# Kernel tuning notes

Hardware: AMD Instinct MI355X
Metric: run time of the kernel (lower is better)

## Reference

```python
import jax, jax.numpy as jnp
import numpy as np
import math

EMB, SEQ, OUT, FF, B = 1024, 1024, 2, 1024, 32
EPS = 1e-5


def _build_pe(seq_len, emb_dim):
    # Faithful to the buggy torch loop: for even i, pe[pos,i] is first set to sin
    # then immediately overwritten by cos(pos / 10000**(2*(i+1)/emb_dim));
    # odd indices are never written (stay 0).
    pos = np.arange(seq_len, dtype=np.float64)[:, None]
    i = np.arange(0, emb_dim, 2, dtype=np.float64)[None, :]
    pe = np.zeros((seq_len, emb_dim), dtype=np.float32)
    pe[:, ::2] = np.cos(pos / 10000.0 ** (2.0 * (i + 1.0) / emb_dim)).astype(np.float32)
    return jnp.asarray(pe)[None]  # [1, S, D]


def setup_inputs() -> dict:
    key = jax.random.key(0)
    ks = jax.random.split(key, 24)
    std = 0.02
    W = lambda k, o, i: jax.random.normal(k, (o, i), jnp.float32) * std
    b = lambda k, o: jax.random.normal(k, (o,), jnp.float32) * std
    return {
        "x": jax.random.normal(ks[0], (B, SEQ, EMB), jnp.float32),
        "pe": _build_pe(SEQ, EMB),
        "ln1_g": jnp.ones((EMB,), jnp.float32), "ln1_b": jnp.zeros((EMB,), jnp.float32),
        "Wq": W(ks[1], EMB, EMB), "bq": b(ks[2], EMB),
        "Wk": W(ks[3], EMB, EMB), "bk": b(ks[4], EMB),
        "Wv": W(ks[5], EMB, EMB), "bv": b(ks[6], EMB),
        "Wo": W(ks[7], EMB, EMB), "bo": b(ks[8], EMB),
        "ln2_g": jnp.ones((EMB,), jnp.float32), "ln2_b": jnp.zeros((EMB,), jnp.float32),
        "W1": W(ks[9], FF, EMB), "b1": b(ks[10], FF),
        "W2": W(ks[11], EMB, FF), "b2": b(ks[12], EMB),
        "Wc": W(ks[13], OUT, EMB), "bc": b(ks[14], OUT),
    }


def _ln(x, g, bias):
    mu = jnp.mean(x, axis=-1, keepdims=True)
    var = jnp.mean(jnp.square(x - mu), axis=-1, keepdims=True)
    return (x - mu) * jax.lax.rsqrt(var + EPS) * g + bias


def _block(x, ln1_g, ln1_b, Wq, bq, Wk, bk, Wv, bv, Wo, bo, ln2_g, ln2_b, W1, b1, W2, b2):
    h = _ln(x, ln1_g, ln1_b)
    q = h @ Wq.T + bq
    k = h @ Wk.T + bk
    v = h @ Wv.T + bv
    scores = jnp.einsum('bqd,bkd->bqk', q, k) / math.sqrt(EMB)
    w = jax.nn.softmax(scores, axis=-1)  # [B,S,S]
    attn = jnp.einsum('bqk,bkd->bqd', w, v) @ Wo.T + bo
    x2 = x + attn  # dropout is identity in eval
    h2 = _ln(x2, ln2_g, ln2_b)
    ff = jax.nn.relu(h2 @ W1.T + b1) @ W2.T + b2
    return x2 + ff, w


def reference(x, pe, ln1_g, ln1_b, Wq, bq, Wk, bk, Wv, bv, Wo, bo, ln2_g, ln2_b, W1, b1, W2, b2, Wc, bc):
    x1 = math.sqrt(EMB) * x + pe
    # Original forward applies block net2_1 twice (net2_2 is unused) -> reuse params.
    p = (ln1_g, ln1_b, Wq, bq, Wk, bk, Wv, bv, Wo, bo, ln2_g, ln2_b, W1, b1, W2, b2)
    x2_1, w1 = _block(x1, *p)
    x2_2, w2 = _block(x2_1, *p)
    logits = x2_2[:, 0, :] @ Wc.T + bc
    return logits, w1, w2
```

## Files before the change

kernel.cpp:

```cpp
#include <hip/hip_runtime.h>
#include <cstdint>


#define AS1 __attribute__((address_space(1)))
#define AS3 __attribute__((address_space(3)))

typedef __attribute__((ext_vector_type(8))) short bf16x8;
typedef __attribute__((ext_vector_type(4))) float f32x4;
typedef __attribute__((ext_vector_type(4))) unsigned short us4;

__device__ __forceinline__ unsigned short f2bf(float f) {
  unsigned int u = __builtin_bit_cast(unsigned int, f);
  u += 0x7fffu + ((u >> 16) & 1u);
  return (unsigned short)(u >> 16);
}
__device__ __forceinline__ float bf2f(unsigned short h) {
  return __builtin_bit_cast(float, (unsigned int)h << 16);
}

__device__ __forceinline__ void gload_lds16(const void* g, void* l) {
  auto gp = reinterpret_cast<AS1 unsigned int*>(reinterpret_cast<uintptr_t>(g));
  auto lp = reinterpret_cast<AS3 unsigned int*>(reinterpret_cast<uintptr_t>(l));
  __builtin_amdgcn_global_load_lds(gp, lp, 16, 0, 0);
}

enum { M_BF16 = 0, M_RELU = 1, M_QKV = 2, M_SCBF = 3, M_RESID = 4 };

template<int MODE>
__global__ __launch_bounds__(256, 3) void gemm_bt(
    const unsigned short* __restrict__ A, long long sAb,
    const unsigned short* __restrict__ B, long long sBb,
    const float* __restrict__ bias,
    const float* __restrict__ resid,
    float* __restrict__ outF,
    unsigned short* __restrict__ outBF,
    long long sOb, int N, int K, float scale)
{
  __shared__ __align__(16) unsigned short As[128 * 64];
  __shared__ __align__(16) unsigned short Bs[128 * 64];
  const int t    = threadIdx.x;
  const int w    = t >> 6;
  const int lane = t & 63;
  const int quad = lane >> 4;
  const int l16  = lane & 15;
  const int bz   = blockIdx.z;
  const unsigned short* Ab = A + (long long)bz * sAb;
  const unsigned short* Bb = B + (long long)bz * sBb;
  const int m0 = blockIdx.y * 128;
  const int n0 = blockIdx.x * 128;
  const int srow = t >> 3;
  const int scol = (t & 7) * 8;
  const int wr = (w >> 1) * 64;
  const int wc = (w & 1) * 64;

  const f32x4 zero = {0.f, 0.f, 0.f, 0.f};
  f32x4 acc[4][4];
#pragma unroll
  for (int i = 0; i < 4; ++i)
#pragma unroll
    for (int j = 0; j < 4; ++j) acc[i][j] = zero;

  for (int k0 = 0; k0 < K; k0 += 64) {
#pragma unroll
    for (int c = 0; c < 4; ++c) {
      gload_lds16(Ab + (long long)(m0 + c * 32 + srow) * K + (k0 + scol),
                  As + c * 2048 + w * 512);
      gload_lds16(Bb + (long long)(n0 + c * 32 + srow) * K + (k0 + scol),
                  Bs + c * 2048 + w * 512);
    }
    __syncthreads();
#pragma unroll
    for (int kk = 0; kk < 64; kk += 32) {
      bf16x8 af[4], bfr[4];
#pragma unroll
      for (int i = 0; i < 4; ++i)
        af[i] = *(const bf16x8*)&As[(wr + i * 16 + l16) * 64 + kk + quad * 8];
#pragma unroll
      for (int j = 0; j < 4; ++j)
        bfr[j] = *(const bf16x8*)&Bs[(wc + j * 16 + l16) * 64 + kk + quad * 8];
#pragma unroll
      for (int i = 0; i < 4; ++i)
#pragma unroll
        for (int j = 0; j < 4; ++j)
          acc[i][j] = __builtin_amdgcn_mfma_f32_16x16x32_bf16(af[i], bfr[j], acc[i][j], 0, 0, 0);
    }
    __syncthreads();
  }

#pragma unroll
  for (int i = 0; i < 4; ++i) {
#pragma unroll
    for (int j = 0; j < 4; ++j) {
      const int mt = m0 + wr + i * 16 + quad * 4;
      const int nt = n0 + wc + j * 16 + l16;
      f32x4 d = acc[i][j];
      if (MODE == M_BF16 || MODE == M_RELU) {
        const float bv = bias ? bias[nt] : 0.0f;
#pragma unroll
        for (int r = 0; r < 4; ++r) {
          float v = d[r] + bv;
          if (MODE == M_RELU) v = fmaxf(v, 0.0f);
          outBF[(long long)bz * sOb + (long long)(mt + r) * N + nt] = f2bf(v);
        }
      } else if (MODE == M_SCBF) {
#pragma unroll
        for (int r = 0; r < 4; ++r)
          outBF[(long long)bz * sOb + (long long)(mt + r) * N + nt] = f2bf(d[r] * scale);
      } else if (MODE == M_RESID) {
        const float bv = bias[nt];
#pragma unroll
        for (int r = 0; r < 4; ++r) {
          const long long idx = (long long)(mt + r) * N + nt;
          outF[idx] = resid[idx] + d[r] + bv;
        }
      } else if (MODE == M_QKV) {
        const int seg = n0 >> 10;
        const int ntl = nt - (seg << 10);
        const float bv = bias[nt];
        if (seg < 2) {
          unsigned short* dst = outBF + (long long)seg * 33554432LL;
#pragma unroll
          for (int r = 0; r < 4; ++r)
            dst[(long long)(mt + r) * 1024 + ntl] = f2bf(d[r] + bv);
        } else {
          unsigned short* dst = outBF + 2LL * 33554432LL;
          us4 pk;
#pragma unroll
          for (int r = 0; r < 4; ++r) pk[r] = f2bf(d[r] + bv);
          const int b = mt >> 10;
          const int s = mt & 1023;
          *(us4*)&dst[(long long)b * 1048576 + (long long)ntl * 1024 + s] = pk;
        }
      }
    }
  }
}

template<int EMBED>
__global__ __launch_bounds__(256) void ln_kernel(
    const float* __restrict__ xin, const float* __restrict__ pe,
    float* __restrict__ x1out,
    const float* __restrict__ g, const float* __restrict__ bb,
    unsigned short* __restrict__ hout)
{
  __shared__ float red[8];
  const long long row = blockIdx.x;
  const int t = threadIdx.x, lane = t & 63, w = t >> 6;
  float4 v = *(const float4*)(xin + row * 1024 + t * 4);
  if (EMBED) {
    const int s = (int)(row & 1023);
    float4 p = *(const float4*)(pe + (long long)s * 1024 + t * 4);
    v.x = 32.0f * v.x + p.x;
    v.y = 32.0f * v.y + p.y;
    v.z = 32.0f * v.z + p.z;
    v.w = 32.0f * v.w + p.w;
    *(float4*)(x1out + row * 1024 + t * 4) = v;
  }
  float sum = v.x + v.y + v.z + v.w;
  float sq  = v.x * v.x + v.y * v.y + v.z * v.z + v.w * v.w;
#pragma unroll
  for (int off = 32; off > 0; off >>= 1) {
    sum += __shfl_down(sum, off, 64);
    sq  += __shfl_down(sq,  off, 64);
  }
  if (lane == 0) { red[w] = sum; red[4 + w] = sq; }
  __syncthreads();
  sum = red[0] + red[1] + red[2] + red[3];
  sq  = red[4] + red[5] + red[6] + red[7];
  const float mu  = sum * (1.0f / 1024.0f);
  const float var = sq * (1.0f / 1024.0f) - mu * mu;
  const float rs  = rsqrtf(var + 1e-5f);
  float4 gg = *(const float4*)(g + t * 4);
  float4 bv = *(const float4*)(bb + t * 4);
  us4 h;
  h[0] = f2bf((v.x - mu) * rs * gg.x + bv.x);
  h[1] = f2bf((v.y - mu) * rs * gg.y + bv.y);
  h[2] = f2bf((v.z - mu) * rs * gg.z + bv.z);
  h[3] = f2bf((v.w - mu) * rs * gg.w + bv.w);
  *(us4*)(hout + row * 1024 + t * 4) = h;
}

__global__ __launch_bounds__(256) void softmax_kernel(
    const unsigned short* __restrict__ sbf,
    float* __restrict__ wout, unsigned short* __restrict__ wbf)
{
  __shared__ float red[8];
  const long long row = blockIdx.x;
  const int t = threadIdx.x, lane = t & 63, w = t >> 6;
  us4 sv = *(const us4*)(sbf + row * 1024 + t * 4);
  float4 v;
  v.x = bf2f(sv[0]); v.y = bf2f(sv[1]); v.z = bf2f(sv[2]); v.w = bf2f(sv[3]);
  float mx = fmaxf(fmaxf(v.x, v.y), fmaxf(v.z, v.w));
#pragma unroll
  for (int off = 32; off > 0; off >>= 1) mx = fmaxf(mx, __shfl_down(mx, off, 64));
  if (lane == 0) red[w] = mx;
  __syncthreads();
  mx = fmaxf(fmaxf(red[0], red[1]), fmaxf(red[2], red[3]));
  __syncthreads();
  const float e0 = __expf(v.x - mx), e1 = __expf(v.y - mx);
  const float e2 = __expf(v.z - mx), e3 = __expf(v.w - mx);
  float s = e0 + e1 + e2 + e3;
#pragma unroll
  for (int off = 32; off > 0; off >>= 1) s += __shfl_down(s, off, 64);
  if (lane == 0) red[w] = s;
  __syncthreads();
  s = red[0] + red[1] + red[2] + red[3];
  const float inv = 1.0f / s;
  float4 o; o.x = e0 * inv; o.y = e1 * inv; o.z = e2 * inv; o.w = e3 * inv;
  *(float4*)(wout + row * 1024 + t * 4) = o;
  us4 ob;
  ob[0] = f2bf(o.x); ob[1] = f2bf(o.y); ob[2] = f2bf(o.z); ob[3] = f2bf(o.w);
  *(us4*)(wbf + row * 1024 + t * 4) = ob;
}

__global__ __launch_bounds__(256) void prep_kernel(
    const float* __restrict__ Wq, const float* __restrict__ Wk, const float* __restrict__ Wv,
    const float* __restrict__ Wo, const float* __restrict__ W1, const float* __restrict__ W2,
    const float* __restrict__ bq, const float* __restrict__ bk, const float* __restrict__ bv,
    unsigned short* __restrict__ qkvw, unsigned short* __restrict__ Wo_bf,
    unsigned short* __restrict__ W1_bf, unsigned short* __restrict__ W2_bf,
    float* __restrict__ qkvb)
{
  const int y = blockIdx.y;
  const long long i = blockIdx.x * 256 + threadIdx.x;
  if (y == 6) {
    if (i < 768) {
      const float* src = (i < 256) ? bq : (i < 512) ? bk : bv;
      float4 v = *(const float4*)(src + (i & 255) * 4);
      *(float4*)(qkvb + i * 4) = v;
    }
    return;
  }
  const float* src;
  unsigned short* dst;
  switch (y) {
    case 0: src = Wq; dst = qkvw;            break;
    case 1: src = Wk; dst = qkvw + 1048576;  break;
    case 2: src = Wv; dst = qkvw + 2097152;  break;
    case 3: src = Wo; dst = Wo_bf;           break;
    case 4: src = W1; dst = W1_bf;           break;
    default: src = W2; dst = W2_bf;          break;
  }
  float4 v = *(const float4*)(src + i * 4);
  us4 o;
  o[0] = f2bf(v.x); o[1] = f2bf(v.y); o[2] = f2bf(v.z); o[3] = f2bf(v.w);
  *(us4*)(dst + i * 4) = o;
}

__global__ __launch_bounds__(256) void logits_kernel(
    const float* __restrict__ x, const float* __restrict__ Wc,
    const float* __restrict__ bc, float* __restrict__ out)
{
  __shared__ float red[4];
  const int blk = blockIdx.x;
  const int b = blk >> 1, o = blk & 1;
  const int t = threadIdx.x, lane = t & 63, w = t >> 6;
  const float* xr = x + (long long)b * 1048576;
  const float* wr = Wc + o * 1024;
  float4 xv = *(const float4*)(xr + t * 4);
  float4 wv = *(const float4*)(wr + t * 4);
  float s = xv.x * wv.x + xv.y * wv.y + xv.z * wv.z + xv.w * wv.w;
#pragma unroll
  for (int off = 32; off > 0; off >>= 1) s += __shfl_down(s, off, 64);
  if (lane == 0) red[w] = s;
  __syncthreads();
  if (t == 0) out[blk] = red[0] + red[1] + red[2] + red[3] + bc[o];
}

extern "C" void kernel_launch(void* const* d_in, const int* in_sizes, int n_in,
                              void* d_out, int out_size, void* d_ws, size_t ws_size,
                              hipStream_t stream)
{
  const float* x    = (const float*)d_in[0];
  const float* pe   = (const float*)d_in[1];
  const float* ln1g = (const float*)d_in[2];
  const float* ln1b = (const float*)d_in[3];
  const float* Wq   = (const float*)d_in[4];
  const float* bq   = (const float*)d_in[5];
  const float* Wk   = (const float*)d_in[6];
  const float* bk   = (const float*)d_in[7];
  const float* Wv   = (const float*)d_in[8];
  const float* bv   = (const float*)d_in[9];
  const float* Wo   = (const float*)d_in[10];
  const float* bo   = (const float*)d_in[11];
  const float* ln2g = (const float*)d_in[12];
  const float* ln2b = (const float*)d_in[13];
  const float* W1   = (const float*)d_in[14];
  const float* b1   = (const float*)d_in[15];
  const float* W2   = (const float*)d_in[16];
  const float* b2   = (const float*)d_in[17];
  const float* Wc   = (const float*)d_in[18];
  const float* bc   = (const float*)d_in[19];
  float* out = (float*)d_out;

  char* ws = (char*)d_ws;
  float*          xbuf  = (float*)ws;
  unsigned short* h_bf  = (unsigned short*)(ws + 134217728LL);
  unsigned short* q_bf  = (unsigned short*)(ws + 134217728LL + 1 * 67108864LL);
  unsigned short* k_bf  = (unsigned short*)(ws + 134217728LL + 2 * 67108864LL);
  unsigned short* vT_bf = (unsigned short*)(ws + 134217728LL + 3 * 67108864LL);
  unsigned short* wts   = (unsigned short*)(ws + 134217728LL + 4 * 67108864LL);
  unsigned short* QKV_bf = wts;
  unsigned short* Wo_bf  = wts + 3LL * 1048576;
  unsigned short* W1_bf  = wts + 4LL * 1048576;
  unsigned short* W2_bf  = wts + 5LL * 1048576;
  float*          qkvb   = (float*)(wts + 6LL * 1048576);
  unsigned short* sc_bf   = h_bf;
  unsigned short* w_bf    = k_bf;
  unsigned short* attn_bf = q_bf;
  unsigned short* ff1_bf  = vT_bf;

  const dim3 blk(256);
  prep_kernel<<<dim3(1024, 7), blk, 0, stream>>>(Wq, Wk, Wv, Wo, W1, W2, bq, bk, bv,
                                                 QKV_bf, Wo_bf, W1_bf, W2_bf, qkvb);

  const dim3 gQKV(24, 256, 1);
  const dim3 gProj(8, 256, 1);
  const dim3 gAttn(8, 8, 32);

  for (int blkI = 0; blkI < 2; ++blkI) {
    float* wslot = out + 64 + (long long)blkI * 33554432LL;

    if (blkI == 0)
      ln_kernel<1><<<32768, blk, 0, stream>>>(x, pe, xbuf, ln1g, ln1b, h_bf);
    else
      ln_kernel<0><<<32768, blk, 0, stream>>>(xbuf, nullptr, nullptr, ln1g, ln1b, h_bf);

    gemm_bt<M_QKV><<<gQKV, blk, 0, stream>>>(h_bf, 0, QKV_bf, 0, qkvb, nullptr,
                                             nullptr, q_bf, 0, 3072, 1024, 1.0f);

    gemm_bt<M_SCBF><<<gAttn, blk, 0, stream>>>(q_bf, 1048576, k_bf, 1048576, nullptr,
                                               nullptr, nullptr, sc_bf, 1048576,
                                               1024, 1024, 0.03125f);
    softmax_kernel<<<32768, blk, 0, stream>>>(sc_bf, wslot, w_bf);

    gemm_bt<M_BF16><<<gAttn, blk, 0, stream>>>(w_bf, 1048576, vT_bf, 1048576, nullptr,
                                               nullptr, nullptr, attn_bf, 1048576,
                                               1024, 1024, 1.0f);
    gemm_bt<M_RESID><<<gProj, blk, 0, stream>>>(attn_bf, 0, Wo_bf, 0, bo, xbuf,
                                                xbuf, nullptr, 0, 1024, 1024, 1.0f);

    ln_kernel<0><<<32768, blk, 0, stream>>>(xbuf, nullptr, nullptr, ln2g, ln2b, h_bf);
    gemm_bt<M_RELU><<<gProj, blk, 0, stream>>>(h_bf, 0, W1_bf, 0, b1, nullptr,
                                               nullptr, ff1_bf, 0, 1024, 1024, 1.0f);
    gemm_bt<M_RESID><<<gProj, blk, 0, stream>>>(ff1_bf, 0, W2_bf, 0, b2, xbuf,
                                                xbuf, nullptr, 0, 1024, 1024, 1.0f);
  }

  logits_kernel<<<64, blk, 0, stream>>>(xbuf, Wc, bc, out);
  (void)in_sizes; (void)n_in; (void)out_size; (void)ws_size;
}
```

Measured before the change: 2.241 ms.

## Rewrite GEMM as 256x256 tile, 8-wave double-buffered pipeline with swizzled LDS

Replaces the 128x128, 4-wave GEMM with a 256x256 tile computed by 8 waves. The K loop is now double-buffered in a 128KB LDS buffer, with async global-to-LDS prefetch of the next K tile interleaved across four MFMA quadrants, explicit barriers and vmcnt waits, and s_setprio raised around MFMA bursts. LDS rows are XOR-swizzled to avoid bank conflicts. This targets memory latency and LDS traffic in all the projection and attention GEMMs. The costs are fewer blocks (grids shrink fourfold), higher register use per thread, and one block per CU because of the LDS size.

New measurement: 1.936 ms. 1.16x faster.

```diff
diff --git a/kernel.cpp b/kernel.cpp
--- a/kernel.cpp
+++ b/kernel.cpp
@@ -26,8 +26,22 @@
 
 enum { M_BF16 = 0, M_RELU = 1, M_QKV = 2, M_SCBF = 3, M_RESID = 4 };
 
+
+#define MFMA_QUAD(qi, qj)                                                          \
+  do {                                                                             \
+    _Pragma("unroll") for (int i2 = 0; i2 < 4; ++i2) {                             \
+      _Pragma("unroll") for (int j2 = 0; j2 < 2; ++j2) {                           \
+        f32x4& c = acc[(qi) * 4 + i2][(qj) * 2 + j2];                              \
+        c = __builtin_amdgcn_mfma_f32_16x16x32_bf16(aF[(qi) * 4 + i2][0],          \
+                                                    bF[(qj) * 2 + j2][0], c, 0, 0, 0); \
+        c = __builtin_amdgcn_mfma_f32_16x16x32_bf16(aF[(qi) * 4 + i2][1],          \
+                                                    bF[(qj) * 2 + j2][1], c, 0, 0, 0); \
+      }                                                                            \
+    }                                                                              \
+  } while (0)
+
 template<int MODE>
-__global__ __launch_bounds__(256, 3) void gemm_bt(
+__global__ __launch_bounds__(512, 2) void gemm_bt(
     const unsigned short* __restrict__ A, long long sAb,
     const unsigned short* __restrict__ B, long long sBb,
     const float* __restrict__ bias,
@@ -36,63 +50,137 @@
     unsigned short* __restrict__ outBF,
     long long sOb, int N, int K, float scale)
 {
-  __shared__ __align__(16) unsigned short As[128 * 64];
-  __shared__ __align__(16) unsigned short Bs[128 * 64];
+  __shared__ __align__(16) unsigned short lds[65536];
   const int t    = threadIdx.x;
   const int w    = t >> 6;
   const int lane = t & 63;
   const int quad = lane >> 4;
   const int l16  = lane & 15;
+  const int l7   = l16 & 7;
+  const int wm   = w >> 2;
+  const int wn   = w & 3;
   const int bz   = blockIdx.z;
   const unsigned short* Ab = A + (long long)bz * sAb;
   const unsigned short* Bb = B + (long long)bz * sBb;
-  const int m0 = blockIdx.y * 128;
-  const int n0 = blockIdx.x * 128;
-  const int srow = t >> 3;
-  const int scol = (t & 7) * 8;
-  const int wr = (w >> 1) * 64;
-  const int wc = (w & 1) * 64;
+  const int m0 = blockIdx.y * 256;
+  const int n0 = blockIdx.x * 256;
+
+  const int sr8  = lane >> 3;
+  const int gseg = ((lane & 7) ^ sr8) << 3;
+  const unsigned short* aSrc = Ab + (long long)(m0 + w * 8 + sr8) * K + gseg;
+  const unsigned short* bSrc = Bb + (long long)(n0 + w * 8 + sr8) * K + gseg;
+  const int ldsW = w << 9;
+
+  const int aOff = (wm * 128 + l16) * 64;
+  const int bOff = 16384 + (wn * 64 + l16) * 64;
+  const int seg0 = (quad ^ l7) << 3;
+  const int seg1 = ((quad + 4) ^ l7) << 3;
+
+  const int NG = K >> 6;
 
   const f32x4 zero = {0.f, 0.f, 0.f, 0.f};
-  f32x4 acc[4][4];
-#pragma unroll
-  for (int i = 0; i < 4; ++i)
+  f32x4 acc[8][4];
+#pragma unroll
+  for (int i = 0; i < 8; ++i)
 #pragma unroll
     for (int j = 0; j < 4; ++j) acc[i][j] = zero;
 
-  for (int k0 = 0; k0 < K; k0 += 64) {
-#pragma unroll
-    for (int c = 0; c < 4; ++c) {
-      gload_lds16(Ab + (long long)(m0 + c * 32 + srow) * K + (k0 + scol),
-                  As + c * 2048 + w * 512);
-      gload_lds16(Bb + (long long)(n0 + c * 32 + srow) * K + (k0 + scol),
-                  Bs + c * 2048 + w * 512);
-    }
-    __syncthreads();
-#pragma unroll
-    for (int kk = 0; kk < 64; kk += 32) {
-      bf16x8 af[4], bfr[4];
-#pragma unroll
-      for (int i = 0; i < 4; ++i)
-        af[i] = *(const bf16x8*)&As[(wr + i * 16 + l16) * 64 + kk + quad * 8];
-#pragma unroll
-      for (int j = 0; j < 4; ++j)
-        bfr[j] = *(const bf16x8*)&Bs[(wc + j * 16 + l16) * 64 + kk + quad * 8];
-#pragma unroll
-      for (int i = 0; i < 4; ++i)
-#pragma unroll
-        for (int j = 0; j < 4; ++j)
-          acc[i][j] = __builtin_amdgcn_mfma_f32_16x16x32_bf16(af[i], bfr[j], acc[i][j], 0, 0, 0);
-    }
-    __syncthreads();
-  }
-
-#pragma unroll
-  for (int i = 0; i < 4; ++i) {
+  bf16x8 aF[8][2];
+  bf16x8 bF[4][2];
+
+#define STAGE_A(kt, h) do {                                                        \
+    const unsigned short* _s = aSrc + (long long)(h) * 128 * K + (kt) * 64;        \
+    unsigned short* _d = &lds[(((kt) & 1) << 15) + ((h) << 13) + ldsW];            \
+    gload_lds16(_s, _d);                                                           \
+    gload_lds16(_s + 64 * (long long)K, _d + 4096);                                \
+  } while (0)
+#define STAGE_B(kt, h) do {                                                        \
+    const unsigned short* _s = bSrc + (long long)(h) * 128 * K + (kt) * 64;        \
+    unsigned short* _d = &lds[(((kt) & 1) << 15) + 16384 + ((h) << 13) + ldsW];    \
+    gload_lds16(_s, _d);                                                           \
+    gload_lds16(_s + 64 * (long long)K, _d + 4096);                                \
+  } while (0)
+
+  STAGE_A(0, 0); STAGE_A(0, 1); STAGE_B(0, 0); STAGE_B(0, 1);
+  STAGE_A(1, 0); STAGE_A(1, 1);
+  asm volatile("s_waitcnt vmcnt(4)" ::: "memory");
+  __builtin_amdgcn_s_barrier();
+  asm volatile("" ::: "memory");
+
+#pragma unroll 1
+  for (int g = 0; g < NG; ++g) {
+    const unsigned short* As = &lds[(g & 1) << 15];
+
+#pragma unroll
+    for (int i2 = 0; i2 < 4; ++i2) {
+      aF[i2][0] = *(const bf16x8*)&As[aOff + i2 * 1024 + seg0];
+      aF[i2][1] = *(const bf16x8*)&As[aOff + i2 * 1024 + seg1];
+    }
+#pragma unroll
+    for (int j2 = 0; j2 < 2; ++j2) {
+      bF[j2][0] = *(const bf16x8*)&As[bOff + j2 * 1024 + seg0];
+      bF[j2][1] = *(const bf16x8*)&As[bOff + j2 * 1024 + seg1];
+    }
+    if (g + 1 < NG) STAGE_B(g + 1, 0);
+    __builtin_amdgcn_s_barrier();
+    asm volatile("s_waitcnt lgkmcnt(0)" ::: "memory");
+    __builtin_amdgcn_s_setprio(1);
+    MFMA_QUAD(0, 0);
+    __builtin_amdgcn_s_setprio(0);
+    __builtin_amdgcn_s_barrier();
+    asm volatile("" ::: "memory");
+
+#pragma unroll
+    for (int i2 = 0; i2 < 4; ++i2) {
+      aF[4 + i2][0] = *(const bf16x8*)&As[aOff + (4 + i2) * 1024 + seg0];
+      aF[4 + i2][1] = *(const bf16x8*)&As[aOff + (4 + i2) * 1024 + seg1];
+    }
+    if (g + 1 < NG) STAGE_B(g + 1, 1);
+    __builtin_amdgcn_s_barrier();
+    asm volatile("s_waitcnt lgkmcnt(0)" ::: "memory");
+    __builtin_amdgcn_s_setprio(1);
+    MFMA_QUAD(1, 0);
+    __builtin_amdgcn_s_setprio(0);
+    __builtin_amdgcn_s_barrier();
+    asm volatile("" ::: "memory");
+
+#pragma unroll
+    for (int j2 = 0; j2 < 2; ++j2) {
+      bF[2 + j2][0] = *(const bf16x8*)&As[bOff + (2 + j2) * 1024 + seg0];
+      bF[2 + j2][1] = *(const bf16x8*)&As[bOff + (2 + j2) * 1024 + seg1];
+    }
+    if (g + 2 < NG) STAGE_A(g + 2, 0);
+    __builtin_amdgcn_s_barrier();
+    asm volatile("s_waitcnt lgkmcnt(0)" ::: "memory");
+    __builtin_amdgcn_s_setprio(1);
+    MFMA_QUAD(1, 1);
+    __builtin_amdgcn_s_setprio(0);
+    __builtin_amdgcn_s_barrier();
+    asm volatile("" ::: "memory");
+
+    if (g + 2 < NG) STAGE_A(g + 2, 1);
+    if (g >= NG - 2) {
+      asm volatile("s_waitcnt vmcnt(0)" ::: "memory");
+    } else {
+      asm volatile("s_waitcnt vmcnt(4)" ::: "memory");
+    }
+    __builtin_amdgcn_s_barrier();
+    __builtin_amdgcn_s_setprio(1);
+    MFMA_QUAD(0, 1);
+    __builtin_amdgcn_s_setprio(0);
+    __builtin_amdgcn_s_barrier();
+    asm volatile("" ::: "memory");
+  }
+
+#undef STAGE_A
+#undef STAGE_B
+
+#pragma unroll
+  for (int i = 0; i < 8; ++i) {
+    const int mt = m0 + wm * 128 + i * 16 + quad * 4;
 #pragma unroll
     for (int j = 0; j < 4; ++j) {
-      const int mt = m0 + wr + i * 16 + quad * 4;
-      const int nt = n0 + wc + j * 16 + l16;
+      const int nt = n0 + wn * 64 + j * 16 + l16;
       f32x4 d = acc[i][j];
       if (MODE == M_BF16 || MODE == M_RELU) {
         const float bv = bias ? bias[nt] : 0.0f;
@@ -311,12 +399,13 @@
   unsigned short* ff1_bf  = vT_bf;
 
   const dim3 blk(256);
+  const dim3 blkG(512);
   prep_kernel<<<dim3(1024, 7), blk, 0, stream>>>(Wq, Wk, Wv, Wo, W1, W2, bq, bk, bv,
                                                  QKV_bf, Wo_bf, W1_bf, W2_bf, qkvb);
 
-  const dim3 gQKV(24, 256, 1);
-  const dim3 gProj(8, 256, 1);
-  const dim3 gAttn(8, 8, 32);
+  const dim3 gQKV(12, 128, 1);
+  const dim3 gProj(4, 128, 1);
+  const dim3 gAttn(4, 4, 32);
 
   for (int blkI = 0; blkI < 2; ++blkI) {
     float* wslot = out + 64 + (long long)blkI * 33554432LL;
@@ -326,25 +415,25 @@
     else
       ln_kernel<0><<<32768, blk, 0, stream>>>(xbuf, nullptr, nullptr, ln1g, ln1b, h_bf);
 
-    gemm_bt<M_QKV><<<gQKV, blk, 0, stream>>>(h_bf, 0, QKV_bf, 0, qkvb, nullptr,
-                                             nullptr, q_bf, 0, 3072, 1024, 1.0f);
-
-    gemm_bt<M_SCBF><<<gAttn, blk, 0, stream>>>(q_bf, 1048576, k_bf, 1048576, nullptr,
-                                               nullptr, nullptr, sc_bf, 1048576,
-                                               1024, 1024, 0.03125f);
+    gemm_bt<M_QKV><<<gQKV, blkG, 0, stream>>>(h_bf, 0, QKV_bf, 0, qkvb, nullptr,
+                                              nullptr, q_bf, 0, 3072, 1024, 1.0f);
+
+    gemm_bt<M_SCBF><<<gAttn, blkG, 0, stream>>>(q_bf, 1048576, k_bf, 1048576, nullptr,
+                                                nullptr, nullptr, sc_bf, 1048576,
+                                                1024, 1024, 0.03125f);
     softmax_kernel<<<32768, blk, 0, stream>>>(sc_bf, wslot, w_bf);
 
-    gemm_bt<M_BF16><<<gAttn, blk, 0, stream>>>(w_bf, 1048576, vT_bf, 1048576, nullptr,
-                                               nullptr, nullptr, attn_bf, 1048576,
-                                               1024, 1024, 1.0f);
-    gemm_bt<M_RESID><<<gProj, blk, 0, stream>>>(attn_bf, 0, Wo_bf, 0, bo, xbuf,
-                                                xbuf, nullptr, 0, 1024, 1024, 1.0f);
+    gemm_bt<M_BF16><<<gAttn, blkG, 0, stream>>>(w_bf, 1048576, vT_bf, 1048576, nullptr,
+                                                nullptr, nullptr, attn_bf, 1048576,
+                                                1024, 1024, 1.0f);
+    gemm_bt<M_RESID><<<gProj, blkG, 0, stream>>>(attn_bf, 0, Wo_bf, 0, bo, xbuf,
+                                                 xbuf, nullptr, 0, 1024, 1024, 1.0f);
 
     ln_kernel<0><<<32768, blk, 0, stream>>>(xbuf, nullptr, nullptr, ln2g, ln2b, h_bf);
-    gemm_bt<M_RELU><<<gProj, blk, 0, stream>>>(h_bf, 0, W1_bf, 0, b1, nullptr,
-                                               nullptr, ff1_bf, 0, 1024, 1024, 1.0f);
-    gemm_bt<M_RESID><<<gProj, blk, 0, stream>>>(ff1_bf, 0, W2_bf, 0, b2, xbuf,
-                                                xbuf, nullptr, 0, 1024, 1024, 1.0f);
+    gemm_bt<M_RELU><<<gProj, blkG, 0, stream>>>(h_bf, 0, W1_bf, 0, b1, nullptr,
+                                                nullptr, ff1_bf, 0, 1024, 1024, 1.0f);
+    gemm_bt<M_RESID><<<gProj, blkG, 0, stream>>>(ff1_bf, 0, W2_bf, 0, b2, xbuf,
+                                                 xbuf, nullptr, 0, 1024, 1024, 1.0f);
   }
 
   logits_kernel<<<64, blk, 0, stream>>>(xbuf, Wc, bc, out);
```
